# Optimization experiments

Hardware: AMD Instinct MI355X
Metric: run time of the kernel (lower is better)

## Reference

```python
import jax, jax.numpy as jnp
import numpy as np

L = 2      # dec_num_layer
B = 32     # batch_size
T = 128    # block_len
H = 128    # dec_num_unit
F = 3      # code_rate_n / code_rate_k
D = 10


def _gru_cell(x, h, Wih, Whh, bih, bhh):
    # PyTorch GRU gate order: r, z, n
    gx = x @ Wih.T + bih
    gh = h @ Whh.T + bhh
    rx, zx, nx = jnp.split(gx, 3, axis=-1)
    rh, zh, nh = jnp.split(gh, 3, axis=-1)
    r = jax.nn.sigmoid(rx + rh)
    z = jax.nn.sigmoid(zx + zh)
    n = jnp.tanh(nx + r * nh)
    return (1.0 - z) * n + z * h


def _gru_stack(x, h, params):
    # x: [B, F], h: [L, B, H]; params: list of (Wih, Whh, bih, bhh) per layer
    hs = []
    inp = x
    for l, (Wih, Whh, bih, bhh) in enumerate(params):
        hl = _gru_cell(inp, h[l], Wih, Whh, bih, bhh)
        hs.append(hl)
        inp = hl
    return jnp.stack(hs), inp  # new hidden [L,B,H], top-layer output [B,H]


def _attend(h_raw, hist, i, attn_W, v_W, fc2_W, fc2_b):
    # h_raw: [L,B,H]; hist: [L,B,T,H]; growing-context attention with mask t<=i
    Ws, Wh = attn_W[:, :H], attn_W[:, H:]
    e = jnp.tanh((h_raw @ Ws.T)[:, :, None, :] + hist @ Wh.T)   # [L,B,T,H]
    logits = jnp.einsum('lbth,h->lbt', e, v_W[0])               # [L,B,T]
    mask = jnp.arange(T) <= i
    logits = jnp.where(mask[None, None, :], logits, -jnp.inf)
    a = jax.nn.softmax(logits, axis=-1)
    c = jnp.einsum('lbt,lbth->lbh', a, hist)                    # [L,B,H]
    return jnp.concatenate([c, h_raw], axis=-1) @ fc2_W.T + fc2_b


def _forward(received, params1, params2, attn_W, v_W, fc2_W, fc2_b, out_W, out_b):
    xs_seq = jnp.transpose(received, (1, 0, 2))  # [T,B,F]

    def step(carry, xs):
        h1, h2, hist1, hist2 = carry
        i, x = xs
        h1_raw, out1 = _gru_stack(x, h1, params1)
        h2_raw, out2 = _gru_stack(x, h2, params2)
        hist1 = hist1.at[:, :, i, :].set(h1_raw)
        hist2 = hist2.at[:, :, i, :].set(h2_raw)
        h1_att = _attend(h1_raw, hist1, i, attn_W, v_W, fc2_W, fc2_b)
        h2_att = _attend(h2_raw, hist2, i, attn_W, v_W, fc2_W, fc2_b)
        # torch skips the attention/fc2 update at step 0
        h1n = jnp.where(i > 0, h1_att, h1_raw)
        h2n = jnp.where(i > 0, h2_att, h2_raw)
        return (h1n, h2n, hist1, hist2), (out1, out2)

    z = jnp.zeros((L, B, H), dtype=received.dtype)
    zh = jnp.zeros((L, B, T, H), dtype=received.dtype)
    _, (o1, o2) = jax.lax.scan(step, (z, z, zh, zh), (jnp.arange(T), xs_seq))
    rnn1 = jnp.transpose(o1, (1, 0, 2))  # [B,T,H]
    rnn2 = jnp.transpose(o2, (1, 0, 2))

    idx = jnp.minimum(jnp.arange(T) + D, T - 1)
    rt_d = rnn2[:, idx, :]
    rnn_out = jnp.concatenate([rnn1, rt_d], axis=-1)            # [B,T,2H]
    dec = jnp.tanh(rnn_out @ out_W.T + out_b)                   # dec_act = tanh
    return jax.nn.sigmoid(dec)                                  # [B,T,1]


def setup_inputs() -> dict:
    key = jax.random.key(0)
    ks = iter(jax.random.split(key, 64))
    s = 0.05
    d = {"received": jax.random.normal(next(ks), (B, T, F), dtype=jnp.float32)}
    for dec in (1, 2):
        for l in range(L):
            inp = F if l == 0 else H
            d[f"Wih{dec}_{l}"] = jax.random.normal(next(ks), (3 * H, inp), dtype=jnp.float32) * s
            d[f"Whh{dec}_{l}"] = jax.random.normal(next(ks), (3 * H, H), dtype=jnp.float32) * s
            d[f"bih{dec}_{l}"] = jax.random.normal(next(ks), (3 * H,), dtype=jnp.float32) * s
            d[f"bhh{dec}_{l}"] = jax.random.normal(next(ks), (3 * H,), dtype=jnp.float32) * s
    d["attn_W"] = jax.random.normal(next(ks), (H, 2 * H), dtype=jnp.float32) * s
    d["v_W"] = jax.random.normal(next(ks), (1, H), dtype=jnp.float32) * s
    d["fc2_W"] = jax.random.normal(next(ks), (H, 2 * H), dtype=jnp.float32) * s
    d["fc2_b"] = jax.random.normal(next(ks), (H,), dtype=jnp.float32) * s
    d["out_W"] = jax.random.normal(next(ks), (1, 2 * H), dtype=jnp.float32) * s
    d["out_b"] = jax.random.normal(next(ks), (1,), dtype=jnp.float32) * s
    return d


def reference(received,
              Wih1_0, Whh1_0, bih1_0, bhh1_0, Wih1_1, Whh1_1, bih1_1, bhh1_1,
              Wih2_0, Whh2_0, bih2_0, bhh2_0, Wih2_1, Whh2_1, bih2_1, bhh2_1,
              attn_W, v_W, fc2_W, fc2_b, out_W, out_b):
    params1 = [(Wih1_0, Whh1_0, bih1_0, bhh1_0), (Wih1_1, Whh1_1, bih1_1, bhh1_1)]
    params2 = [(Wih2_0, Whh2_0, bih2_0, bhh2_0), (Wih2_1, Whh2_1, bih2_1, bhh2_1)]
    return _forward(received, params1, params2, attn_W, v_W, fc2_W, fc2_b, out_W, out_b)
```

## Files before the change

### kernel.cpp

```cpp
#include <hip/hip_runtime.h>

typedef _Float16 half_t;
typedef __attribute__((ext_vector_type(2))) _Float16 half2_t;

__device__ __forceinline__ half2_t bc2(unsigned int u){ return __builtin_bit_cast(half2_t, u); }
__device__ __forceinline__ float fdot2f(half2_t a, half2_t b, float c){
  return __builtin_amdgcn_fdot2(a, b, c, false);
}
__device__ __forceinline__ float rcp_f(float x){ return __builtin_amdgcn_rcpf(x); }
__device__ __forceinline__ float sigmoidf_(float x){ return rcp_f(1.0f+__expf(-x)); }
__device__ __forceinline__ float tanhf_(float x){ return 1.0f - 2.0f*rcp_f(__expf(2.0f*x)+1.0f); }

__device__ __forceinline__ float qxor1(float v){
  return __builtin_bit_cast(float, __builtin_amdgcn_mov_dpp(__builtin_bit_cast(int,v),0xB1,0xF,0xF,true));
}
__device__ __forceinline__ float qxor2(float v){
  return __builtin_bit_cast(float, __builtin_amdgcn_mov_dpp(__builtin_bit_cast(int,v),0x4E,0xF,0xF,true));
}
__device__ __forceinline__ float qsum4(float v){ v += qxor1(v); v += qxor2(v); return v; }

__device__ __forceinline__ void bar(){
  asm volatile("s_waitcnt lgkmcnt(0)\n\ts_barrier" ::: "memory");
}

__device__ __forceinline__ float dot32(const uint4* w, const uint4* x){
  float a=0.f,b=0.f,c=0.f,d=0.f;
  #pragma unroll
  for (int m=0;m<4;++m){
    a=fdot2f(bc2(w[m].x),bc2(x[m].x),a);
    b=fdot2f(bc2(w[m].y),bc2(x[m].y),b);
    c=fdot2f(bc2(w[m].z),bc2(x[m].z),c);
    d=fdot2f(bc2(w[m].w),bc2(x[m].w),d);
  }
  return (a+b)+(c+d);
}

template<int L>
__device__ __forceinline__ void phase6(int i, int tid,
    const half_t* shWh, const half_t* sWs0, const half_t* sWs1,
    const half_t* vw, float* probs0, float* probs1)
{
  const int sub = tid & (L-1);
  const int pid = tid / L;
  const int t6  = (L==2) ? (pid & 127) : (L==4) ? (pid & 63) : (pid & 31);
  const int l6  = (L==2) ? (pid >> 7)  : (L==4) ? (pid >> 6) : (pid >> 5);
  if (t6 <= i){
    const half_t* hwrow = shWh + (size_t)l6*(128*136) + t6*136;
    const half_t* swrow = l6 ? sWs1 : sWs0;
    const int M  = 16/L;
    const int m0 = M*sub;
    const int key = t6 & 15;
    float s = 0.f;
    #pragma unroll
    for (int mm=0; mm<M; ++mm){
      int m = m0+mm;
      uint4 hw = *reinterpret_cast<const uint4*>(hwrow + ((m^key)*8));
      uint4 sw = *reinterpret_cast<const uint4*>(swrow + 8*m);
      uint4 vv = *reinterpret_cast<const uint4*>(vw + 8*m);
      half2_t h2,s2,v2;
      h2=bc2(hw.x); s2=bc2(sw.x); v2=bc2(vv.x);
      s += tanhf_((float)s2[0]+(float)h2[0])*(float)v2[0];
      s += tanhf_((float)s2[1]+(float)h2[1])*(float)v2[1];
      h2=bc2(hw.y); s2=bc2(sw.y); v2=bc2(vv.y);
      s += tanhf_((float)s2[0]+(float)h2[0])*(float)v2[0];
      s += tanhf_((float)s2[1]+(float)h2[1])*(float)v2[1];
      h2=bc2(hw.z); s2=bc2(sw.z); v2=bc2(vv.z);
      s += tanhf_((float)s2[0]+(float)h2[0])*(float)v2[0];
      s += tanhf_((float)s2[1]+(float)h2[1])*(float)v2[1];
      h2=bc2(hw.w); s2=bc2(sw.w); v2=bc2(vv.w);
      s += tanhf_((float)s2[0]+(float)h2[0])*(float)v2[0];
      s += tanhf_((float)s2[1]+(float)h2[1])*(float)v2[1];
    }
    s += qxor1(s);
    if (L>=4) s += qxor2(s);
    if (L>=8) s += __shfl_xor(s,4);
    if (sub==0) (l6 ? probs1 : probs0)[t6] = __expf(s - 4.0f);
  }
}

__global__ void pack_k(const float* __restrict__ src, half_t* __restrict__ dst,
                       int R, int K, int ld, int coloff, int RT, int row_off){
  int idx = blockIdx.x*blockDim.x + threadIdx.x;
  if (idx >= R*K) return;
  int r = idx / K, k = idx - r*K;
  int kc = k >> 3, j = k & 7;
  dst[((size_t)kc*RT + row_off + r)*8 + j] = (half_t)src[(size_t)r*ld + coloff + k];
}

__launch_bounds__(512)
__global__ void gru_main(
    const float* __restrict__ received,
    const float* __restrict__ Wih0d0, const float* __restrict__ Wih0d1,
    const float* __restrict__ bx0d0, const float* __restrict__ bh0d0,
    const float* __restrict__ bx1d0, const float* __restrict__ bh1d0,
    const float* __restrict__ bx0d1, const float* __restrict__ bh0d1,
    const float* __restrict__ bx1d1, const float* __restrict__ bh1d1,
    const float* __restrict__ vW, const float* __restrict__ fc2b,
    const half_t* __restrict__ W0pack, const half_t* __restrict__ W1pack,
    const half_t* __restrict__ WsPack, const half_t* __restrict__ WhPack,
    const half_t* __restrict__ fc2Pack,
    half_t* __restrict__ o1h, half_t* __restrict__ o2h)
{
  const int dec = blockIdx.x >> 5;
  const int b   = blockIdx.x & 31;
  const int tid = threadIdx.x;
  const int q   = tid & 3;
  const int r   = tid >> 2;

  const float* bx0  = dec ? bx0d1 : bx0d0;
  const float* bh0  = dec ? bh0d1 : bh0d0;
  const float* bx1  = dec ? bx1d1 : bx1d0;
  const float* bh1  = dec ? bh1d1 : bh1d0;
  const float* Wih0 = dec ? Wih0d1 : Wih0d0;
  const half_t* W0  = W0pack + (size_t)dec*49152;
  const half_t* W1  = W1pack + (size_t)dec*98304;
  half_t* od = dec ? o2h : o1h;

  __shared__ __align__(16) half_t sh_hist[2][128*136];
  __shared__ __align__(16) half_t sh_histWh[2][128*136];
  __shared__ __align__(16) float  sh_gx[384];
  __shared__ __align__(16) float  sh_gh[384];
  __shared__ __align__(16) float  sh_g1x[384];
  __shared__ __align__(16) float  sh_g1h[384];
  __shared__ __align__(16) half_t sh_sWs16[2][128];
  __shared__ __align__(16) float  sh_probs[2][128];
  __shared__ __align__(16) float  sh_hatt32[2][128];
  __shared__ __align__(16) half_t sh_hatt_pk[2][128];
  __shared__ __align__(16) float  sh_hraw32[2][128];
  __shared__ __align__(16) half_t sh_hraw_pk[2][128];
  __shared__ __align__(16) half_t sh_fc2in[2][256];
  __shared__ __align__(16) half_t sh_vW16[128];
  __shared__ __align__(16) float4 sh_Wx4[384];

  float bA=0.f,bB=0.f,bC=0.f;
  if (q==0){ bA=bh0[r];     bB=bh1[r+128]; bC=bx1[r];     }
  else if (q==1){ bA=bh0[r+128]; bB=bh1[r+256]; bC=bx1[r+128]; }
  else if (q==2){ bA=bh0[r+256];                bC=bx1[r+256]; }
  else { bB=bh1[r]; }
  const float bF = fc2b[r];

  {
    uint4 z = make_uint4(0u,0u,0u,0u);
    uint4* ph = reinterpret_cast<uint4*>(&sh_hist[0][0]);
    uint4* pw = reinterpret_cast<uint4*>(&sh_histWh[0][0]);
    for (int j=tid; j<4352; j+=512){ ph[j]=z; pw[j]=z; }
  }
  if (tid < 256){ int l=tid>>7, rr=tid&127; sh_hatt32[l][rr]=0.f; sh_hatt_pk[l][rr]=(half_t)0.f; }
  if (tid < 128) sh_vW16[tid] = (half_t)vW[tid];
  if (tid < 384) sh_Wx4[tid] = make_float4(Wih0[tid*3], Wih0[tid*3+1], Wih0[tid*3+2], bx0[tid]);
  bar();

  for (int i=0; i<128; ++i){
    {
      uint4 xa[4];
      #pragma unroll
      for (int m=0;m<4;++m) xa[m] = *reinterpret_cast<const uint4*>(&sh_hatt_pk[0][32*q+8*m]);
      float a0,a1,a2;
      {
        uint4 w[12];
        #pragma unroll
        for (int n=0;n<3;++n)
          #pragma unroll
          for (int m=0;m<4;++m)
            w[4*n+m] = *reinterpret_cast<const uint4*>(W0 + ((size_t)(4*q+m)*384 + r + 128*n)*8);
        a0 = dot32(&w[0],xa); a1 = dot32(&w[4],xa); a2 = dot32(&w[8],xa);
      }
      __builtin_amdgcn_sched_barrier(0);
      uint4 xb[4];
      #pragma unroll
      for (int m=0;m<4;++m) xb[m] = *reinterpret_cast<const uint4*>(&sh_hatt_pk[1][32*q+8*m]);
      float a3,a4,a5;
      {
        uint4 w[12];
        #pragma unroll
        for (int n=0;n<3;++n)
          #pragma unroll
          for (int m=0;m<4;++m)
            w[4*n+m] = *reinterpret_cast<const uint4*>(W1 + ((size_t)(4*q+m)*768 + 384 + r + 128*n)*8);
        a3 = dot32(&w[0],xb); a4 = dot32(&w[4],xb); a5 = dot32(&w[8],xb);
      }
      a0=qsum4(a0); a1=qsum4(a1); a2=qsum4(a2);
      a3=qsum4(a3); a4=qsum4(a4); a5=qsum4(a5);
      if      (q==0){ sh_gh[r]      = a0+bA; sh_g1h[r+128] = a4+bB; }
      else if (q==1){ sh_gh[r+128]  = a1+bA; sh_g1h[r+256] = a5+bB; }
      else if (q==2){ sh_gh[r+256]  = a2+bA; }
      else          { sh_g1h[r]     = a3+bB; }
      if (tid < 384){
        const float* xr = &received[((size_t)b*128+i)*3];
        float4 wx = sh_Wx4[tid];
        sh_gx[tid] = wx.w + wx.x*xr[0] + wx.y*xr[1] + wx.z*xr[2];
      }
    }
    bar();
    if (tid < 128){
      float rr = sigmoidf_(sh_gx[tid]+sh_gh[tid]);
      float zz = sigmoidf_(sh_gx[128+tid]+sh_gh[128+tid]);
      float nn = tanhf_(sh_gx[256+tid] + rr*sh_gh[256+tid]);
      float h0 = (1.f-zz)*nn + zz*sh_hatt32[0][tid];
      sh_hraw32[0][tid]=h0;
      half_t hh=(half_t)h0;
      sh_hist[0][i*136 + ((tid>>3)^(i&15))*8 + (tid&7)] = hh;
      sh_hraw_pk[0][tid]=hh; sh_fc2in[0][128+tid]=hh;
    }
    bar();
    {
      uint4 xc[4];
      #pragma unroll
      for (int m=0;m<4;++m) xc[m] = *reinterpret_cast<const uint4*>(&sh_hraw_pk[0][32*q+8*m]);
      uint4 w[12];
      #pragma unroll
      for (int n=0;n<3;++n)
        #pragma unroll
        for (int m=0;m<4;++m)
          w[4*n+m] = *reinterpret_cast<const uint4*>(W1 + ((size_t)(4*q+m)*768 + r + 128*n)*8);
      float a0 = dot32(&w[0],xc), a1 = dot32(&w[4],xc), a2 = dot32(&w[8],xc);
      a0=qsum4(a0); a1=qsum4(a1); a2=qsum4(a2);
      if      (q==0) sh_g1x[r]     = a0+bC;
      else if (q==1) sh_g1x[r+128] = a1+bC;
      else if (q==2) sh_g1x[r+256] = a2+bC;
    }
    bar();
    if (tid < 128){
      float rr = sigmoidf_(sh_g1x[tid]+sh_g1h[tid]);
      float zz = sigmoidf_(sh_g1x[128+tid]+sh_g1h[128+tid]);
      float nn = tanhf_(sh_g1x[256+tid] + rr*sh_g1h[256+tid]);
      float h1 = (1.f-zz)*nn + zz*sh_hatt32[1][tid];
      sh_hraw32[1][tid]=h1;
      half_t hh=(half_t)h1;
      sh_hist[1][i*136 + ((tid>>3)^(i&15))*8 + (tid&7)] = hh;
      sh_hraw_pk[1][tid]=hh; sh_fc2in[1][128+tid]=hh;
      od[(size_t)(b*128+i)*128 + tid] = hh;
    }
    bar();
    {
      uint4 xa[4], xb[4], ws[4], wh[4];
      #pragma unroll
      for (int m=0;m<4;++m){
        xa[m] = *reinterpret_cast<const uint4*>(&sh_hraw_pk[0][32*q+8*m]);
        xb[m] = *reinterpret_cast<const uint4*>(&sh_hraw_pk[1][32*q+8*m]);
        ws[m] = *reinterpret_cast<const uint4*>(WsPack + ((size_t)(4*q+m)*128 + r)*8);
        wh[m] = *reinterpret_cast<const uint4*>(WhPack + ((size_t)(4*q+m)*128 + r)*8);
      }
      float sA0=qsum4(dot32(ws,xa));
      float sA1=qsum4(dot32(ws,xb));
      float sB0=qsum4(dot32(wh,xa));
      float sB1=qsum4(dot32(wh,xb));
      int phys = i*136 + ((r>>3)^(i&15))*8 + (r&7);
      if      (q==0) sh_sWs16[0][r] = (half_t)sA0;
      else if (q==1) sh_sWs16[1][r] = (half_t)sA1;
      else if (q==2) sh_histWh[0][phys] = (half_t)sB0;
      else           sh_histWh[1][phys] = (half_t)sB1;
    }
    bar();
    if (i > 0){
      if (i < 32)      phase6<8>(i, tid, &sh_histWh[0][0], &sh_sWs16[0][0], &sh_sWs16[1][0], &sh_vW16[0], &sh_probs[0][0], &sh_probs[1][0]);
      else if (i < 64) phase6<4>(i, tid, &sh_histWh[0][0], &sh_sWs16[0][0], &sh_sWs16[1][0], &sh_vW16[0], &sh_probs[0][0], &sh_probs[1][0]);
      else             phase6<2>(i, tid, &sh_histWh[0][0], &sh_sWs16[0][0], &sh_sWs16[1][0], &sh_vW16[0], &sh_probs[0][0], &sh_probs[1][0]);
      if (tid < 256){ int l=tid>>7, t=tid&127; if (t > i) sh_probs[l][t] = 0.f; }
      bar();
      uint4 wE[8];
      #pragma unroll
      for (int c=0;c<8;++c)
        wE[c] = *reinterpret_cast<const uint4*>(fc2Pack + ((size_t)(8*q+c)*128 + r)*8);
      {
        int ts=tid&15, oc=(tid>>4)&15, l8=tid>>8;
        float c0=0.f,c1=0.f,c2=0.f,c3=0.f,c4=0.f,c5=0.f,c6=0.f,c7=0.f, ps=0.f;
        int kmax = (i>>4)+1;
        for (int k=0;k<kmax;++k){
          int t = ts + 16*k;
          float p = sh_probs[l8][t];
          uint4 hv = *reinterpret_cast<const uint4*>(&sh_hist[l8][t*136 + ((oc^(t&15))*8)]);
          half2_t a=bc2(hv.x), e=bc2(hv.y), f=bc2(hv.z), g=bc2(hv.w);
          c0+=p*(float)a[0]; c1+=p*(float)a[1]; c2+=p*(float)e[0]; c3+=p*(float)e[1];
          c4+=p*(float)f[0]; c5+=p*(float)f[1]; c6+=p*(float)g[0]; c7+=p*(float)g[1];
          ps+=p;
        }
        c0+=qxor1(c0); c0+=qxor2(c0);  c1+=qxor1(c1); c1+=qxor2(c1);
        c2+=qxor1(c2); c2+=qxor2(c2);  c3+=qxor1(c3); c3+=qxor2(c3);
        c4+=qxor1(c4); c4+=qxor2(c4);  c5+=qxor1(c5); c5+=qxor2(c5);
        c6+=qxor1(c6); c6+=qxor2(c6);  c7+=qxor1(c7); c7+=qxor2(c7);
        ps+=qxor1(ps); ps+=qxor2(ps);
        c0+=__shfl_xor(c0,4); c1+=__shfl_xor(c1,4); c2+=__shfl_xor(c2,4); c3+=__shfl_xor(c3,4);
        c4+=__shfl_xor(c4,4); c5+=__shfl_xor(c5,4); c6+=__shfl_xor(c6,4); c7+=__shfl_xor(c7,4);
        ps+=__shfl_xor(ps,4);
        c0+=__shfl_xor(c0,8); c1+=__shfl_xor(c1,8); c2+=__shfl_xor(c2,8); c3+=__shfl_xor(c3,8);
        c4+=__shfl_xor(c4,8); c5+=__shfl_xor(c5,8); c6+=__shfl_xor(c6,8); c7+=__shfl_xor(c7,8);
        ps+=__shfl_xor(ps,8);
        if (ts==0){
          float inv = rcp_f(ps);
          half2_t o01={(half_t)(c0*inv),(half_t)(c1*inv)};
          half2_t o23={(half_t)(c2*inv),(half_t)(c3*inv)};
          half2_t o45={(half_t)(c4*inv),(half_t)(c5*inv)};
          half2_t o67={(half_t)(c6*inv),(half_t)(c7*inv)};
          *reinterpret_cast<uint4*>(&sh_fc2in[l8][oc*8]) =
              make_uint4((unsigned)__builtin_bit_cast(int,o01),(unsigned)__builtin_bit_cast(int,o23),
                         (unsigned)__builtin_bit_cast(int,o45),(unsigned)__builtin_bit_cast(int,o67));
        }
      }
      bar();
      {
        float e0=0.f, e1=0.f;
        #pragma unroll
        for (int h=0; h<2; ++h){
          uint4 x0[4], x1[4];
          #pragma unroll
          for (int m=0;m<4;++m){
            x0[m] = *reinterpret_cast<const uint4*>(&sh_fc2in[0][64*q + 32*h + 8*m]);
            x1[m] = *reinterpret_cast<const uint4*>(&sh_fc2in[1][64*q + 32*h + 8*m]);
          }
          e0 += dot32(&wE[4*h],x0);
          e1 += dot32(&wE[4*h],x1);
        }
        e0 = qsum4(e0); e1 = qsum4(e1);
        if      (q==0){ float v=e0+bF; sh_hatt32[0][r]=v; sh_hatt_pk[0][r]=(half_t)v; }
        else if (q==1){ float v=e1+bF; sh_hatt32[1][r]=v; sh_hatt_pk[1][r]=(half_t)v; }
      }
    } else {
      if (tid < 256){
        int l=tid>>7, row=tid&127;
        float hv = sh_hraw32[l][row];
        sh_hatt32[l][row]=hv; sh_hatt_pk[l][row]=(half_t)hv;
      }
    }
    bar();
  }
}

__global__ void out_kernel(const half_t* __restrict__ o1h, const half_t* __restrict__ o2h,
                           const float* __restrict__ outW, const float* __restrict__ outb,
                           float* __restrict__ dout){
  int tid = blockIdx.x*blockDim.x + threadIdx.x;
  int q = tid&3, job = tid>>2;
  int b = job>>7, t = job&127;
  int t2 = t+10; if (t2>127) t2=127;
  const half_t* r1 = o1h + (size_t)(b*128+t)*128;
  const half_t* r2 = o2h + (size_t)(b*128+t2)*128;
  float acc=0.f;
  for (int j=q*32; j<q*32+32; ++j) acc += outW[j]*(float)r1[j];
  for (int j=q*32; j<q*32+32; ++j) acc += outW[128+j]*(float)r2[j];
  acc += __shfl_xor(acc,1);
  acc += __shfl_xor(acc,2);
  if (q==0){
    float d = tanhf_(acc + outb[0]);
    dout[job] = rcp_f(1.f+__expf(-d));
  }
}

static inline void launch_pack(const void* src, half_t* dst, int R, int K, int ld,
                               int coloff, int RT, int row_off, hipStream_t s){
  int total = R*K;
  pack_k<<<(total+255)/256, 256, 0, s>>>((const float*)src, dst, R, K, ld, coloff, RT, row_off);
}

extern "C" void kernel_launch(void* const* d_in, const int* in_sizes, int n_in,
                              void* d_out, int out_size, void* d_ws, size_t ws_size,
                              hipStream_t stream) {
  const float* received = (const float*)d_in[0];
  const float* Wih1_0 = (const float*)d_in[1];
  const float* Whh1_0 = (const float*)d_in[2];
  const float* bih1_0 = (const float*)d_in[3];
  const float* bhh1_0 = (const float*)d_in[4];
  const float* Wih1_1 = (const float*)d_in[5];
  const float* Whh1_1 = (const float*)d_in[6];
  const float* bih1_1 = (const float*)d_in[7];
  const float* bhh1_1 = (const float*)d_in[8];
  const float* Wih2_0 = (const float*)d_in[9];
  const float* Whh2_0 = (const float*)d_in[10];
  const float* bih2_0 = (const float*)d_in[11];
  const float* bhh2_0 = (const float*)d_in[12];
  const float* Wih2_1 = (const float*)d_in[13];
  const float* Whh2_1 = (const float*)d_in[14];
  const float* bih2_1 = (const float*)d_in[15];
  const float* bhh2_1 = (const float*)d_in[16];
  const float* attn_W = (const float*)d_in[17];
  const float* v_W    = (const float*)d_in[18];
  const float* fc2_W  = (const float*)d_in[19];
  const float* fc2_b  = (const float*)d_in[20];
  const float* out_W  = (const float*)d_in[21];
  const float* out_b  = (const float*)d_in[22];

  half_t* ws = (half_t*)d_ws;
  half_t* W0pack  = ws + 0;
  half_t* W1pack  = ws + 98304;
  half_t* WsPack  = ws + 294912;
  half_t* WhPack  = ws + 311296;
  half_t* fc2Pack = ws + 327552;
  half_t* o1h     = ws + 360448;
  half_t* o2h     = ws + 884736;

  launch_pack(Whh1_0, W0pack,          384, 128, 128, 0, 384, 0, stream);
  launch_pack(Whh2_0, W0pack + 49152,  384, 128, 128, 0, 384, 0, stream);
  launch_pack(Wih1_1, W1pack,          384, 128, 128, 0, 768, 0, stream);
  launch_pack(Whh1_1, W1pack,          384, 128, 128, 0, 768, 384, stream);
  launch_pack(Wih2_1, W1pack + 98304,  384, 128, 128, 0, 768, 0, stream);
  launch_pack(Whh2_1, W1pack + 98304,  384, 128, 128, 0, 768, 384, stream);
  launch_pack(attn_W, WsPack,          128, 128, 256, 0,   128, 0, stream);
  launch_pack(attn_W, WhPack,          128, 128, 256, 128, 128, 0, stream);
  launch_pack(fc2_W,  fc2Pack,         128, 256, 256, 0,   128, 0, stream);

  gru_main<<<64, 512, 0, stream>>>(
      received,
      Wih1_0, Wih2_0,
      bih1_0, bhh1_0, bih1_1, bhh1_1,
      bih2_0, bhh2_0, bih2_1, bhh2_1,
      v_W, fc2_b,
      W0pack, W1pack, WsPack, WhPack, fc2Pack,
      o1h, o2h);

  out_kernel<<<64, 256, 0, stream>>>(o1h, o2h, out_W, out_b, (float*)d_out);
}
```

Baseline: 1.407 ms.

## Software-prefetch per-phase weight tiles one phase ahead across barriers

Weight loads for each phase of the recurrent step (layer-0 hidden weights, layer-1 input weights, attention Ws/Wh) are now issued during the preceding phase into persistent register arrays. The goal is to hide global/L2 load latency behind barriers and earlier compute instead of stalling at the start of each phase. This raises register pressure (about 32 extra uint4 live across barriers), which could reduce occupancy or cause spills.

```diff
diff --git a/kernel.cpp b/kernel.cpp
--- a/kernel.cpp
+++ b/kernel.cpp
@@ -139,6 +139,10 @@
   else { bB=bh1[r]; }
   const float bF = fc2b[r];
 
+  uint4 wP1[12];
+  uint4 wP3[12];
+  uint4 wP5[8];
+
   {
     uint4 z = make_uint4(0u,0u,0u,0u);
     uint4* ph = reinterpret_cast<uint4*>(&sh_hist[0][0]);
@@ -148,37 +152,35 @@
   if (tid < 256){ int l=tid>>7, rr=tid&127; sh_hatt32[l][rr]=0.f; sh_hatt_pk[l][rr]=(half_t)0.f; }
   if (tid < 128) sh_vW16[tid] = (half_t)vW[tid];
   if (tid < 384) sh_Wx4[tid] = make_float4(Wih0[tid*3], Wih0[tid*3+1], Wih0[tid*3+2], bx0[tid]);
+  #pragma unroll
+  for (int n=0;n<3;++n)
+    #pragma unroll
+    for (int m=0;m<4;++m)
+      wP1[4*n+m] = *reinterpret_cast<const uint4*>(W0 + ((size_t)(4*q+m)*384 + r + 128*n)*8);
   bar();
 
   for (int i=0; i<128; ++i){
     {
+      uint4 w1[12];
+      #pragma unroll
+      for (int n=0;n<3;++n)
+        #pragma unroll
+        for (int m=0;m<4;++m)
+          w1[4*n+m] = *reinterpret_cast<const uint4*>(W1 + ((size_t)(4*q+m)*768 + 384 + r + 128*n)*8);
       uint4 xa[4];
       #pragma unroll
       for (int m=0;m<4;++m) xa[m] = *reinterpret_cast<const uint4*>(&sh_hatt_pk[0][32*q+8*m]);
-      float a0,a1,a2;
-      {
-        uint4 w[12];
+      float a0 = dot32(&wP1[0],xa), a1 = dot32(&wP1[4],xa), a2 = dot32(&wP1[8],xa);
+      uint4 xb[4];
+      #pragma unroll
+      for (int m=0;m<4;++m) xb[m] = *reinterpret_cast<const uint4*>(&sh_hatt_pk[1][32*q+8*m]);
+      float a3 = dot32(&w1[0],xb), a4 = dot32(&w1[4],xb), a5 = dot32(&w1[8],xb);
+      __builtin_amdgcn_sched_barrier(0);
+      #pragma unroll
+      for (int n=0;n<3;++n)
         #pragma unroll
-        for (int n=0;n<3;++n)
-          #pragma unroll
-          for (int m=0;m<4;++m)
-            w[4*n+m] = *reinterpret_cast<const uint4*>(W0 + ((size_t)(4*q+m)*384 + r + 128*n)*8);
-        a0 = dot32(&w[0],xa); a1 = dot32(&w[4],xa); a2 = dot32(&w[8],xa);
-      }
-      __builtin_amdgcn_sched_barrier(0);
-      uint4 xb[4];
-      #pragma unroll
-      for (int m=0;m<4;++m) xb[m] = *reinterpret_cast<const uint4*>(&sh_hatt_pk[1][32*q+8*m]);
-      float a3,a4,a5;
-      {
-        uint4 w[12];
-        #pragma unroll
-        for (int n=0;n<3;++n)
-          #pragma unroll
-          for (int m=0;m<4;++m)
-            w[4*n+m] = *reinterpret_cast<const uint4*>(W1 + ((size_t)(4*q+m)*768 + 384 + r + 128*n)*8);
-        a3 = dot32(&w[0],xb); a4 = dot32(&w[4],xb); a5 = dot32(&w[8],xb);
-      }
+        for (int m=0;m<4;++m)
+          wP3[4*n+m] = *reinterpret_cast<const uint4*>(W1 + ((size_t)(4*q+m)*768 + r + 128*n)*8);
       a0=qsum4(a0); a1=qsum4(a1); a2=qsum4(a2);
       a3=qsum4(a3); a4=qsum4(a4); a5=qsum4(a5);
       if      (q==0){ sh_gh[r]      = a0+bA; sh_g1h[r+128] = a4+bB; }
@@ -207,13 +209,13 @@
       uint4 xc[4];
       #pragma unroll
       for (int m=0;m<4;++m) xc[m] = *reinterpret_cast<const uint4*>(&sh_hraw_pk[0][32*q+8*m]);
-      uint4 w[12];
-      #pragma unroll
-      for (int n=0;n<3;++n)
-        #pragma unroll
-        for (int m=0;m<4;++m)
-          w[4*n+m] = *reinterpret_cast<const uint4*>(W1 + ((size_t)(4*q+m)*768 + r + 128*n)*8);
-      float a0 = dot32(&w[0],xc), a1 = dot32(&w[4],xc), a2 = dot32(&w[8],xc);
+      float a0 = dot32(&wP3[0],xc), a1 = dot32(&wP3[4],xc), a2 = dot32(&wP3[8],xc);
+      __builtin_amdgcn_sched_barrier(0);
+      #pragma unroll
+      for (int m=0;m<4;++m){
+        wP5[m]   = *reinterpret_cast<const uint4*>(WsPack + ((size_t)(4*q+m)*128 + r)*8);
+        wP5[4+m] = *reinterpret_cast<const uint4*>(WhPack + ((size_t)(4*q+m)*128 + r)*8);
+      }
       a0=qsum4(a0); a1=qsum4(a1); a2=qsum4(a2);
       if      (q==0) sh_g1x[r]     = a0+bC;
       else if (q==1) sh_g1x[r+128] = a1+bC;
@@ -233,18 +235,16 @@
     }
     bar();
     {
-      uint4 xa[4], xb[4], ws[4], wh[4];
+      uint4 xa[4], xb[4];
       #pragma unroll
       for (int m=0;m<4;++m){
         xa[m] = *reinterpret_cast<const uint4*>(&sh_hraw_pk[0][32*q+8*m]);
         xb[m] = *reinterpret_cast<const uint4*>(&sh_hraw_pk[1][32*q+8*m]);
-        ws[m] = *reinterpret_cast<const uint4*>(WsPack + ((size_t)(4*q+m)*128 + r)*8);
-        wh[m] = *reinterpret_cast<const uint4*>(WhPack + ((size_t)(4*q+m)*128 + r)*8);
-      }
-      float sA0=qsum4(dot32(ws,xa));
-      float sA1=qsum4(dot32(ws,xb));
-      float sB0=qsum4(dot32(wh,xa));
-      float sB1=qsum4(dot32(wh,xb));
+      }
+      float sA0=qsum4(dot32(&wP5[0],xa));
+      float sA1=qsum4(dot32(&wP5[0],xb));
+      float sB0=qsum4(dot32(&wP5[4],xa));
+      float sB1=qsum4(dot32(&wP5[4],xb));
       int phys = i*136 + ((r>>3)^(i&15))*8 + (r&7);
       if      (q==0) sh_sWs16[0][r] = (half_t)sA0;
       else if (q==1) sh_sWs16[1][r] = (half_t)sA1;
@@ -312,10 +312,21 @@
           e1 += dot32(&wE[4*h],x1);
         }
         e0 = qsum4(e0); e1 = qsum4(e1);
+        __builtin_amdgcn_sched_barrier(0);
+        #pragma unroll
+        for (int n=0;n<3;++n)
+          #pragma unroll
+          for (int m=0;m<4;++m)
+            wP1[4*n+m] = *reinterpret_cast<const uint4*>(W0 + ((size_t)(4*q+m)*384 + r + 128*n)*8);
         if      (q==0){ float v=e0+bF; sh_hatt32[0][r]=v; sh_hatt_pk[0][r]=(half_t)v; }
         else if (q==1){ float v=e1+bF; sh_hatt32[1][r]=v; sh_hatt_pk[1][r]=(half_t)v; }
       }
     } else {
+      #pragma unroll
+      for (int n=0;n<3;++n)
+        #pragma unroll
+        for (int m=0;m<4;++m)
+          wP1[4*n+m] = *reinterpret_cast<const uint4*>(W0 + ((size_t)(4*q+m)*384 + r + 128*n)*8);
       if (tid < 256){
         int l=tid>>7, row=tid&127;
         float hv = sh_hraw32[l][row];
```

New measurement: 1.319 ms. 6.2% less time.
